# Kernel optimization log

Hardware: AMD Instinct MI355X
Metric: run time of the kernel (lower is better)

Reference implementation:

```python
import jax, jax.numpy as jnp
import numpy as np

N = 50000      # nodes
E = 800000     # edges (before self-loops)
F_IN = 128     # num_features
H = 4          # heads
C = 64         # hidden_channels
HC = H * C     # 256
NEG_SLOPE = 0.2


def setup_inputs() -> dict:
    key = jax.random.key(0)
    ks = jax.random.split(key, 20)
    x = jax.random.normal(ks[0], (N, F_IN), dtype=jnp.float32)
    edge_index = jax.random.randint(ks[1], (2, E), 0, N, dtype=jnp.int32)
    s = 0.05
    inp = {"x": x, "edge_index": edge_index}
    dims_in = [F_IN, HC, HC, HC]
    for l in range(4):
        kW, ka, kb = jax.random.split(ks[2 + l], 3)
        inp[f"W{l+1}"] = jax.random.normal(kW, (dims_in[l], HC), dtype=jnp.float32) * s
        inp[f"a_src{l+1}"] = jax.random.normal(ka, (H, C), dtype=jnp.float32) * s
        inp[f"a_dst{l+1}"] = jax.random.normal(kb, (H, C), dtype=jnp.float32) * s
        inp[f"b{l+1}"] = jnp.zeros((HC,), dtype=jnp.float32)
    return inp


def gat_conv(x, src, dst, W, a_src, a_dst, b):
    # x: [N, F_in] -> h: [N, H, C]
    h = (x @ W).reshape(N, H, C)
    es = jnp.sum(h * a_src, axis=-1)  # [N, H] per-node source logits
    ed = jnp.sum(h * a_dst, axis=-1)  # [N, H]
    e = jax.nn.leaky_relu(es[src] + ed[dst], NEG_SLOPE)  # [Etot, H]
    m = jax.ops.segment_max(e, dst, num_segments=N)      # per-dst max
    m = jnp.where(jnp.isfinite(m), m, 0.0)
    ex = jnp.exp(e - m[dst])
    denom = jax.ops.segment_sum(ex, dst, num_segments=N)
    alpha = ex / (denom[dst] + 1e-16)                     # edge softmax
    out = jax.ops.segment_sum(alpha[:, :, None] * h[src], dst, num_segments=N)
    return out.reshape(N, HC) + b


def reference(x, edge_index,
              W1, a_src1, a_dst1, b1,
              W2, a_src2, a_dst2, b2,
              W3, a_src3, a_dst3, b3,
              W4, a_src4, a_dst4, b4):
    loop = jnp.arange(N, dtype=edge_index.dtype)
    src = jnp.concatenate([edge_index[0], loop])  # add self-loops (PyG default)
    dst = jnp.concatenate([edge_index[1], loop])
    x1 = jax.nn.relu(gat_conv(x, src, dst, W1, a_src1, a_dst1, b1))
    x2 = jax.nn.relu(gat_conv(x1, src, dst, W2, a_src2, a_dst2, b2))
    x3 = jax.nn.relu(gat_conv(x2 + x1, src, dst, W3, a_src3, a_dst3, b3))
    x4 = jax.nn.relu(gat_conv(x2 + x3, src, dst, W4, a_src4, a_dst4, b4))
    # NOTE: source code calls conv4 again (not conv5) -- reproduced faithfully
    x5 = gat_conv(x4 + x3, src, dst, W4, a_src4, a_dst4, b4)
    return x5
```

## Files before the change

### kernel.cpp

```cpp
#include <hip/hip_runtime.h>
#include <hip/hip_bf16.h>

#define N_NODES 50000
#define E_EDGES 800000
#define ETOT (E_EDGES + N_NODES)
#define HC 256
#define NHEAD 4
#define CHAN 64
#define NEG 0.2f
#define NBLK ((N_NODES + 1023) / 1024)

typedef _Float16 half8 __attribute__((ext_vector_type(8)));
typedef _Float16 half4v __attribute__((ext_vector_type(4)));
typedef float float4v __attribute__((ext_vector_type(4)));


__global__ void count_kernel(const int* __restrict__ ei, int* __restrict__ counts) {
    int i = blockIdx.x * blockDim.x + threadIdx.x;
    if (i >= ETOT) return;
    int dst = (i < E_EDGES) ? ei[E_EDGES + i] : (i - E_EDGES);
    atomicAdd(&counts[dst], 1);
}

__global__ __launch_bounds__(256) void blocksum_kernel(const int* __restrict__ counts,
                                                       int* __restrict__ blocksums) {
    __shared__ int s[4];
    int b = blockIdx.x, tid = threadIdx.x;
    int base = b * 1024;
    int sum = 0;
    #pragma unroll
    for (int r = 0; r < 4; ++r) {
        int idx = base + r * 256 + tid;
        sum += (idx < N_NODES) ? counts[idx] : 0;
    }
    #pragma unroll
    for (int m = 1; m < 64; m <<= 1) sum += __shfl_xor(sum, m, 64);
    if ((tid & 63) == 0) s[tid >> 6] = sum;
    __syncthreads();
    if (tid == 0) blocksums[b] = s[0] + s[1] + s[2] + s[3];
}

__global__ __launch_bounds__(64) void blockscan_kernel(int* __restrict__ blocksums) {
    int tid = threadIdx.x;
    int v = (tid < NBLK) ? blocksums[tid] : 0;
    #pragma unroll
    for (int off = 1; off < 64; off <<= 1) {
        int t = __shfl_up(v, off, 64);
        if (tid >= off) v += t;
    }
    if (tid < NBLK) blocksums[tid] = v;
}

__global__ __launch_bounds__(1024) void scatter_scan_kernel(const int* __restrict__ counts,
                                                            const int* __restrict__ blocksums,
                                                            int* __restrict__ offsets,
                                                            int* __restrict__ cursor) {
    __shared__ int s[1024];
    int b = blockIdx.x, tid = threadIdx.x;
    int idx = b * 1024 + tid;
    int v = (idx < N_NODES) ? counts[idx] : 0;
    s[tid] = v;
    __syncthreads();
    for (int off = 1; off < 1024; off <<= 1) {
        int t = (tid >= off) ? s[tid - off] : 0;
        __syncthreads();
        s[tid] += t;
        __syncthreads();
    }
    int excl = s[tid] - v + (b > 0 ? blocksums[b - 1] : 0);
    if (idx < N_NODES) { offsets[idx] = excl; cursor[idx] = excl; }
    if (idx == N_NODES - 1) offsets[N_NODES] = excl + v;
}

__global__ void fill_kernel(const int* __restrict__ ei, int* __restrict__ cursor,
                            int* __restrict__ csr_src, int* __restrict__ csr_dst) {
    int i = blockIdx.x * blockDim.x + threadIdx.x;
    if (i >= ETOT) return;
    int src, dst;
    if (i < E_EDGES) { src = ei[i]; dst = ei[E_EDGES + i]; }
    else             { src = i - E_EDGES; dst = src; }
    int pos = atomicAdd(&cursor[dst], 1);
    csr_src[pos] = src;
    csr_dst[pos] = dst;
}


__global__ void wsplit_kernel(const float* __restrict__ W, _Float16* __restrict__ Wth,
                              _Float16* __restrict__ Wtl, int K) {
    int id = blockIdx.x * 256 + threadIdx.x;
    if (id >= K * 256) return;
    int n = id & 255, k = id >> 8;
    float w = W[(size_t)k * 256 + n];
    _Float16 h = (_Float16)w;
    _Float16 l = (_Float16)(w - (float)h);
    Wth[(size_t)n * K + k] = h;
    Wtl[(size_t)n * K + k] = l;
}

__global__ void xsplit_kernel(const float* __restrict__ x, _Float16* __restrict__ xh,
                              _Float16* __restrict__ xl, int total) {
    int id = blockIdx.x * 256 + threadIdx.x;
    if (id >= total) return;
    float v = x[id];
    _Float16 h = (_Float16)v;
    xh[id] = h;
    xl[id] = (_Float16)(v - (float)h);
}


__global__ __launch_bounds__(256) void edge_alpha_kernel(
        const float* __restrict__ es, const float* __restrict__ ed,
        const int* __restrict__ csr_src, const int* __restrict__ csr_dst,
        float* __restrict__ ex) {
    int e = blockIdx.x * 256 + threadIdx.x;
    if (e >= ETOT) return;
    int s = csr_src[e], d = csr_dst[e];
    float4 esv = *(const float4*)(es + (size_t)s * 4);
    float4 edv = *(const float4*)(ed + (size_t)d * 4);
    float4 v;
    v.x = esv.x + edv.x; v.y = esv.y + edv.y;
    v.z = esv.z + edv.z; v.w = esv.w + edv.w;
    v.x = (v.x > 0.f) ? v.x : NEG * v.x;
    v.y = (v.y > 0.f) ? v.y : NEG * v.y;
    v.z = (v.z > 0.f) ? v.z : NEG * v.z;
    v.w = (v.w > 0.f) ? v.w : NEG * v.w;
    v.x = __expf(v.x); v.y = __expf(v.y);
    v.z = __expf(v.z); v.w = __expf(v.w);
    *(float4*)(ex + (size_t)e * 4) = v;
}


template<int K, bool HASLO, bool HAS2>
__global__ __launch_bounds__(256) void gemm_mfma_kernel(
        const _Float16* __restrict__ A1h, const _Float16* __restrict__ A1l,
        const _Float16* __restrict__ A2h,
        const _Float16* __restrict__ Wth, const _Float16* __restrict__ Wtl,
        const float* __restrict__ a_src, const float* __restrict__ a_dst,
        _Float16* __restrict__ H16, float* __restrict__ es, float* __restrict__ ed,
        int M) {
    constexpr int LDA = K + 16;
    constexpr int NC  = K / 32;
    constexpr int CPR = K / 8;
    __shared__ _Float16 Ah[64][LDA];
    __shared__ _Float16 Al[HASLO ? 64 : 1][HASLO ? LDA : 8];
    __shared__ _Float16 Bh[256][40];
    __shared__ _Float16 Bl[256][40];

    int tid = threadIdx.x;
    int m0 = blockIdx.x * 64;
    int w = tid >> 6, lane = tid & 63;
    int rn = w * 64;
    int fr = lane & 15;
    int q  = lane >> 4;
    int fk = q * 8;

    int wr = tid >> 2;
    int wk = (tid & 3) * 8;

    half8 a1c[NC], a2c[HAS2 ? NC : 1], alc[HASLO ? NC : 1];
    #pragma unroll
    for (int c = 0; c < NC; ++c) {
        int idx = c * 256 + tid;
        int row = idx / CPR, col = (idx % CPR) * 8;
        int grow = m0 + row;
        a1c[c] = (half8)(_Float16)0;
        if (grow < M) a1c[c] = *(const half8*)(A1h + (size_t)grow * K + col);
        if constexpr (HAS2) {
            a2c[c] = (half8)(_Float16)0;
            if (grow < M) a2c[c] = *(const half8*)(A2h + (size_t)grow * K + col);
        }
        if constexpr (HASLO) {
            alc[c] = (half8)(_Float16)0;
            if (grow < M) alc[c] = *(const half8*)(A1l + (size_t)grow * K + col);
        }
    }
    half8 pbh[4], pbl[4];
    auto loadB = [&](int k0) {
        #pragma unroll
        for (int g = 0; g < 4; ++g) {
            int r = g * 64 + wr;
            pbh[g] = *(const half8*)(Wth + (size_t)r * K + k0 + wk);
            pbl[g] = *(const half8*)(Wtl + (size_t)r * K + k0 + wk);
        }
    };
    loadB(0);

    #pragma unroll
    for (int c = 0; c < NC; ++c) {
        int idx = c * 256 + tid;
        int row = idx / CPR, col = (idx % CPR) * 8;
        half8 v = a1c[c];
        if constexpr (HAS2) v = v + a2c[c];
        *(half8*)&Ah[row][col] = v;
        if constexpr (HASLO) *(half8*)&Al[row][col] = alc[c];
    }

    float4v acc[4][4];
    #pragma unroll
    for (int i = 0; i < 4; ++i)
        #pragma unroll
        for (int j = 0; j < 4; ++j)
            acc[i][j] = (float4v){0.f, 0.f, 0.f, 0.f};

    __syncthreads();

    for (int kk = 0; kk < K / 32; ++kk) {
        int k0 = kk * 32;
        #pragma unroll
        for (int g = 0; g < 4; ++g) {
            int r = g * 64 + wr;
            *(half8*)&Bh[r][wk] = pbh[g];
            *(half8*)&Bl[r][wk] = pbl[g];
        }
        __syncthreads();
        if (kk + 1 < K / 32) loadB(k0 + 32);
        half8 afh[4], bfh[4], bfl[4];
        #pragma unroll
        for (int t = 0; t < 4; ++t) {
            afh[t] = *(const half8*)&Ah[t * 16 + fr][k0 + fk];
            bfh[t] = *(const half8*)&Bh[rn + t * 16 + fr][fk];
            bfl[t] = *(const half8*)&Bl[rn + t * 16 + fr][fk];
        }
        if constexpr (HASLO) {
            half8 afl[4];
            #pragma unroll
            for (int t = 0; t < 4; ++t) afl[t] = *(const half8*)&Al[t * 16 + fr][k0 + fk];
            #pragma unroll
            for (int tm = 0; tm < 4; ++tm)
                #pragma unroll
                for (int tn = 0; tn < 4; ++tn)
                    acc[tm][tn] = __builtin_amdgcn_mfma_f32_16x16x32_f16(
                        afl[tm], bfh[tn], acc[tm][tn], 0, 0, 0);
        }
        #pragma unroll
        for (int tm = 0; tm < 4; ++tm)
            #pragma unroll
            for (int tn = 0; tn < 4; ++tn) {
                float4v c = acc[tm][tn];
                c = __builtin_amdgcn_mfma_f32_16x16x32_f16(afh[tm], bfl[tn], c, 0, 0, 0);
                c = __builtin_amdgcn_mfma_f32_16x16x32_f16(afh[tm], bfh[tn], c, 0, 0, 0);
                acc[tm][tn] = c;
            }
        __syncthreads();
    }

    float asv[4], adv[4];
    #pragma unroll
    for (int tn = 0; tn < 4; ++tn) {
        asv[tn] = a_src[w * CHAN + tn * 16 + fr];
        adv[tn] = a_dst[w * CHAN + tn * 16 + fr];
    }
    #pragma unroll
    for (int tm = 0; tm < 4; ++tm) {
        #pragma unroll
        for (int i = 0; i < 4; ++i) {
            int row = m0 + tm * 16 + q * 4 + i;
            float ps = 0.f, pd = 0.f;
            #pragma unroll
            for (int tn = 0; tn < 4; ++tn) {
                float hv = acc[tm][tn][i];
                ps += hv * asv[tn];
                pd += hv * adv[tn];
                if (row < M)
                    H16[(size_t)row * HC + rn + tn * 16 + fr] = (_Float16)hv;
            }
            #pragma unroll
            for (int msk = 1; msk < 16; msk <<= 1) {
                ps += __shfl_xor(ps, msk, 64);
                pd += __shfl_xor(pd, msk, 64);
            }
            if (fr == 0 && row < M) {
                es[row * NHEAD + w] = ps;
                ed[row * NHEAD + w] = pd;
            }
        }
    }
}


__global__ __launch_bounds__(256) void gat_aggregate_kernel(
        const _Float16* __restrict__ H16, const float* __restrict__ ex,
        const int* __restrict__ offsets, const int* __restrict__ csr_src,
        const float* __restrict__ bias, _Float16* __restrict__ out16,
        float* __restrict__ out32, int do_relu) {
    __shared__ float ex_lds[4][256];
    __shared__ int   src_lds[4][64];
    int tid = threadIdx.x;
    int w = tid >> 6, lane = tid & 63;
    int n = blockIdx.x * 4 + w;
    int off = offsets[n];
    int deg = offsets[n + 1] - off;

    if (deg <= 64) {
        int sreg = n;
        float4 ex4 = make_float4(0.f, 0.f, 0.f, 0.f);
        if (lane < deg) {
            sreg = csr_src[off + lane];
            ex4 = *(const float4*)(ex + (size_t)(off + lane) * 4);
        }
        src_lds[w][lane] = sreg;
        *(float4*)&ex_lds[w][lane * 4] = ex4;

        int hl = lane & 31, side = lane >> 5;
        int hd = hl >> 3;
        float av[8] = {0.f, 0.f, 0.f, 0.f, 0.f, 0.f, 0.f, 0.f};
        int degr = (deg + 7) & ~7;
        #pragma unroll 2
        for (int j0 = 0; j0 < degr; j0 += 8) {
            int j = j0 + side;
            int s0 = src_lds[w][j];
            int s1 = src_lds[w][j + 2];
            int s2 = src_lds[w][j + 4];
            int s3 = src_lds[w][j + 6];
            float w0 = ex_lds[w][j * 4 + hd];
            float w1 = ex_lds[w][(j + 2) * 4 + hd];
            float w2 = ex_lds[w][(j + 4) * 4 + hd];
            float w3 = ex_lds[w][(j + 6) * 4 + hd];
            half8 h0 = *(const half8*)(H16 + (size_t)s0 * HC + hl * 8);
            half8 h1 = *(const half8*)(H16 + (size_t)s1 * HC + hl * 8);
            half8 h2 = *(const half8*)(H16 + (size_t)s2 * HC + hl * 8);
            half8 h3 = *(const half8*)(H16 + (size_t)s3 * HC + hl * 8);
            #pragma unroll
            for (int c = 0; c < 8; ++c) {
                av[c] += w0 * (float)h0[c];
                av[c] += w1 * (float)h1[c];
                av[c] += w2 * (float)h2[c];
                av[c] += w3 * (float)h3[c];
            }
        }

        float4 l4 = ex4;
        #pragma unroll
        for (int msk = 1; msk < 64; msk <<= 1) {
            l4.x += __shfl_xor(l4.x, msk, 64);
            l4.y += __shfl_xor(l4.y, msk, 64);
            l4.z += __shfl_xor(l4.z, msk, 64);
            l4.w += __shfl_xor(l4.w, msk, 64);
        }
        #pragma unroll
        for (int c = 0; c < 8; ++c) av[c] += __shfl_xor(av[c], 32, 64);
        if (side == 0) {
            float denom = (hd == 0) ? l4.x : (hd == 1) ? l4.y : (hd == 2) ? l4.z : l4.w;
            float scale = 1.f / (denom + 1e-16f);
            float4 b0 = *(const float4*)(bias + hl * 8);
            float4 b1 = *(const float4*)(bias + hl * 8 + 4);
            float o[8] = {av[0] * scale + b0.x, av[1] * scale + b0.y,
                          av[2] * scale + b0.z, av[3] * scale + b0.w,
                          av[4] * scale + b1.x, av[5] * scale + b1.y,
                          av[6] * scale + b1.z, av[7] * scale + b1.w};
            if (do_relu)
                #pragma unroll
                for (int c = 0; c < 8; ++c) o[c] = fmaxf(o[c], 0.f);
            if (out16) {
                half8 ov = {(_Float16)o[0], (_Float16)o[1], (_Float16)o[2], (_Float16)o[3],
                            (_Float16)o[4], (_Float16)o[5], (_Float16)o[6], (_Float16)o[7]};
                *(half8*)(out16 + (size_t)n * HC + hl * 8) = ov;
            } else {
                *(float4*)(out32 + (size_t)n * HC + hl * 8) =
                    make_float4(o[0], o[1], o[2], o[3]);
                *(float4*)(out32 + (size_t)n * HC + hl * 8 + 4) =
                    make_float4(o[4], o[5], o[6], o[7]);
            }
        }
        return;
    }

    int head = lane >> 4;
    float4 acc0 = make_float4(0.f, 0.f, 0.f, 0.f);
    float den = 0.f;
    for (int j = 0; j < deg; ++j) {
        int s = csr_src[off + j];
        float exv = ex[(size_t)(off + j) * 4 + head];
        den += exv;
        half4v h0 = *(const half4v*)(H16 + (size_t)s * HC + lane * 4);
        acc0.x += exv * (float)h0[0]; acc0.y += exv * (float)h0[1];
        acc0.z += exv * (float)h0[2]; acc0.w += exv * (float)h0[3];
    }
    float scale = 1.f / (den + 1e-16f);
    float4 b4 = *(const float4*)(bias + lane * 4);
    float o[4] = {acc0.x * scale + b4.x, acc0.y * scale + b4.y,
                  acc0.z * scale + b4.z, acc0.w * scale + b4.w};
    if (do_relu)
        #pragma unroll
        for (int c = 0; c < 4; ++c) o[c] = fmaxf(o[c], 0.f);
    if (out16) {
        half4v ov = {(_Float16)o[0], (_Float16)o[1], (_Float16)o[2], (_Float16)o[3]};
        *(half4v*)(out16 + (size_t)n * HC + lane * 4) = ov;
    } else {
        *(float4*)(out32 + (size_t)n * HC + lane * 4) = make_float4(o[0], o[1], o[2], o[3]);
    }
}


extern "C" void kernel_launch(void* const* d_in, const int* in_sizes, int n_in,
                              void* d_out, int out_size, void* d_ws, size_t ws_size,
                              hipStream_t stream) {
    const float* x  = (const float*)d_in[0];
    const int*   ei = (const int*)d_in[1];
    const float *W[5], *Asrc[5], *Adst[5], *Bs[5];
    for (int l = 0; l < 4; ++l) {
        W[l]    = (const float*)d_in[2 + l * 4];
        Asrc[l] = (const float*)d_in[3 + l * 4];
        Adst[l] = (const float*)d_in[4 + l * 4];
        Bs[l]   = (const float*)d_in[5 + l * 4];
    }
    W[4] = W[3]; Asrc[4] = Asrc[3]; Adst[4] = Adst[3]; Bs[4] = Bs[3];

    char* ws = (char*)d_ws;
    size_t off = 0;
    auto alloc = [&](size_t bytes) -> void* {
        void* p = ws + off;
        off += (bytes + 255) & ~(size_t)255;
        return p;
    };
    _Float16* h16  = (_Float16*)alloc((size_t)N_NODES * HC * 2);
    _Float16* xa   = (_Float16*)alloc((size_t)N_NODES * HC * 2);
    _Float16* xb   = (_Float16*)alloc((size_t)N_NODES * HC * 2);
    _Float16* xc   = (_Float16*)alloc((size_t)N_NODES * HC * 2);
    _Float16* xd   = (_Float16*)alloc((size_t)N_NODES * HC * 2);
    _Float16* xh   = (_Float16*)alloc((size_t)N_NODES * 128 * 2);
    _Float16* xl   = (_Float16*)alloc((size_t)N_NODES * 128 * 2);
    float* es      = (float*)alloc((size_t)N_NODES * 4 * 4);
    float* ed      = (float*)alloc((size_t)N_NODES * 4 * 4);
    float* exbuf   = (float*)alloc((size_t)ETOT * 4 * 4);
    int*   counts  = (int*)alloc((size_t)N_NODES * 4);
    int*   offsets = (int*)alloc((size_t)(N_NODES + 1) * 4);
    int*   cursor  = (int*)alloc((size_t)N_NODES * 4);
    int*   csr_src = (int*)alloc((size_t)ETOT * 4);
    int*   csr_dst = (int*)alloc((size_t)ETOT * 4);
    int*   blocksums = (int*)alloc((size_t)NBLK * 4);
    _Float16 *Wth[5], *Wtl[5];
    int Ks[4] = {128, 256, 256, 256};
    for (int l = 0; l < 4; ++l) {
        Wth[l] = (_Float16*)alloc((size_t)256 * Ks[l] * 2);
        Wtl[l] = (_Float16*)alloc((size_t)256 * Ks[l] * 2);
    }
    Wth[4] = Wth[3]; Wtl[4] = Wtl[3];

    hipMemsetAsync(counts, 0, (size_t)N_NODES * 4, stream);
    count_kernel<<<(ETOT + 255) / 256, 256, 0, stream>>>(ei, counts);
    blocksum_kernel<<<NBLK, 256, 0, stream>>>(counts, blocksums);
    blockscan_kernel<<<1, 64, 0, stream>>>(blocksums);
    scatter_scan_kernel<<<NBLK, 1024, 0, stream>>>(counts, blocksums, offsets, cursor);
    fill_kernel<<<(ETOT + 255) / 256, 256, 0, stream>>>(ei, cursor, csr_src, csr_dst);
    for (int l = 0; l < 4; ++l)
        wsplit_kernel<<<(Ks[l] * 256 + 255) / 256, 256, 0, stream>>>(W[l], Wth[l], Wtl[l], Ks[l]);
    xsplit_kernel<<<(N_NODES * 128 + 255) / 256, 256, 0, stream>>>(x, xh, xl, N_NODES * 128);

    int gemm_grid = (N_NODES + 63) / 64;
    auto agg = [&](int l, _Float16* o16, float* o32, int relu) {
        edge_alpha_kernel<<<(ETOT + 255) / 256, 256, 0, stream>>>(
            es, ed, csr_src, csr_dst, exbuf);
        gat_aggregate_kernel<<<N_NODES / 4, 256, 0, stream>>>(
            h16, exbuf, offsets, csr_src, Bs[l], o16, o32, relu);
    };

    float* out = (float*)d_out;
    gemm_mfma_kernel<128, true, false><<<gemm_grid, 256, 0, stream>>>(
        xh, xl, nullptr, Wth[0], Wtl[0], Asrc[0], Adst[0], h16, es, ed, N_NODES);
    agg(0, xa, nullptr, 1);
    gemm_mfma_kernel<256, false, false><<<gemm_grid, 256, 0, stream>>>(
        xa, nullptr, nullptr, Wth[1], Wtl[1], Asrc[1], Adst[1], h16, es, ed, N_NODES);
    agg(1, xb, nullptr, 1);
    gemm_mfma_kernel<256, false, true><<<gemm_grid, 256, 0, stream>>>(
        xb, nullptr, xa, Wth[2], Wtl[2], Asrc[2], Adst[2], h16, es, ed, N_NODES);
    agg(2, xc, nullptr, 1);
    gemm_mfma_kernel<256, false, true><<<gemm_grid, 256, 0, stream>>>(
        xb, nullptr, xc, Wth[3], Wtl[3], Asrc[3], Adst[3], h16, es, ed, N_NODES);
    agg(3, xd, nullptr, 1);
    gemm_mfma_kernel<256, false, true><<<gemm_grid, 256, 0, stream>>>(
        xd, nullptr, xc, Wth[4], Wtl[4], Asrc[4], Adst[4], h16, es, ed, N_NODES);
    agg(4, nullptr, out, 0);
}
```

Measured before the change: 753.6 us.

## Stage GEMM output through LDS for coalesced stores; split aggregate launch in halves

```diff
diff --git a/kernel.cpp b/kernel.cpp
--- a/kernel.cpp
+++ b/kernel.cpp
@@ -130,6 +130,19 @@
 }
 
 
+template<int K, bool HASLO>
+struct SmemLayout {
+    _Float16 Ah[64][K + 8];
+    _Float16 Al[HASLO ? 64 : 1][HASLO ? (K + 8) : 8];
+    _Float16 Bh[256][40];
+    _Float16 Bl[256][40];
+};
+template<int K, bool HASLO>
+union SmemU {
+    SmemLayout<K, HASLO> t;
+    _Float16 out[64][264];
+};
+
 template<int K, bool HASLO, bool HAS2>
 __global__ __launch_bounds__(256) void gemm_mfma_kernel(
         const _Float16* __restrict__ A1h, const _Float16* __restrict__ A1l,
@@ -138,13 +151,13 @@
         const float* __restrict__ a_src, const float* __restrict__ a_dst,
         _Float16* __restrict__ H16, float* __restrict__ es, float* __restrict__ ed,
         int M) {
-    constexpr int LDA = K + 16;
     constexpr int NC  = K / 32;
     constexpr int CPR = K / 8;
-    __shared__ _Float16 Ah[64][LDA];
-    __shared__ _Float16 Al[HASLO ? 64 : 1][HASLO ? LDA : 8];
-    __shared__ _Float16 Bh[256][40];
-    __shared__ _Float16 Bl[256][40];
+    __shared__ SmemU<K, HASLO> u;
+    auto& Ah = u.t.Ah;
+    auto& Al = u.t.Al;
+    auto& Bh = u.t.Bh;
+    auto& Bl = u.t.Bl;
 
     int tid = threadIdx.x;
     int m0 = blockIdx.x * 64;
@@ -254,27 +267,38 @@
     for (int tm = 0; tm < 4; ++tm) {
         #pragma unroll
         for (int i = 0; i < 4; ++i) {
-            int row = m0 + tm * 16 + q * 4 + i;
+            int r = tm * 16 + q * 4 + i;
             float ps = 0.f, pd = 0.f;
             #pragma unroll
             for (int tn = 0; tn < 4; ++tn) {
                 float hv = acc[tm][tn][i];
                 ps += hv * asv[tn];
                 pd += hv * adv[tn];
-                if (row < M)
-                    H16[(size_t)row * HC + rn + tn * 16 + fr] = (_Float16)hv;
+                u.out[r][rn + tn * 16 + fr] = (_Float16)hv;
             }
             #pragma unroll
             for (int msk = 1; msk < 16; msk <<= 1) {
                 ps += __shfl_xor(ps, msk, 64);
                 pd += __shfl_xor(pd, msk, 64);
             }
+            int row = m0 + r;
             if (fr == 0 && row < M) {
                 es[row * NHEAD + w] = ps;
                 ed[row * NHEAD + w] = pd;
             }
         }
     }
+    __syncthreads();
+
+    #pragma unroll
+    for (int k = 0; k < 8; ++k) {
+        int c = k * 256 + tid;
+        int r = c >> 5, cc = c & 31;
+        if (m0 + r < M) {
+            half8 v = *(const half8*)(&u.out[r][0] + cc * 8);
+            *(half8*)(H16 + (size_t)(m0 + r) * HC + cc * 8) = v;
+        }
+    }
 }
 
 
@@ -282,12 +306,12 @@
         const _Float16* __restrict__ H16, const float* __restrict__ ex,
         const int* __restrict__ offsets, const int* __restrict__ csr_src,
         const float* __restrict__ bias, _Float16* __restrict__ out16,
-        float* __restrict__ out32, int do_relu) {
+        float* __restrict__ out32, int do_relu, int node_base) {
     __shared__ float ex_lds[4][256];
     __shared__ int   src_lds[4][64];
     int tid = threadIdx.x;
     int w = tid >> 6, lane = tid & 63;
-    int n = blockIdx.x * 4 + w;
+    int n = node_base + blockIdx.x * 4 + w;
     int off = offsets[n];
     int deg = offsets[n + 1] - off;
 
@@ -451,8 +475,10 @@
     auto agg = [&](int l, _Float16* o16, float* o32, int relu) {
         edge_alpha_kernel<<<(ETOT + 255) / 256, 256, 0, stream>>>(
             es, ed, csr_src, csr_dst, exbuf);
-        gat_aggregate_kernel<<<N_NODES / 4, 256, 0, stream>>>(
-            h16, exbuf, offsets, csr_src, Bs[l], o16, o32, relu);
+        gat_aggregate_kernel<<<N_NODES / 8, 256, 0, stream>>>(
+            h16, exbuf, offsets, csr_src, Bs[l], o16, o32, relu, 0);
+        gat_aggregate_kernel<<<N_NODES / 8, 256, 0, stream>>>(
+            h16, exbuf, offsets, csr_src, Bs[l], o16, o32, relu, N_NODES / 2);
     };
 
     float* out = (float*)d_out;
```

Result: slower. 770.0 us (+2.2%).
